# Performance work log

Measured on AMD Instinct MI355X. Metric: run time of the kernel, lower is better.

The kernel has to match this reference:

```python
import jax, jax.numpy as jnp
import numpy as np

B, T, V, E, H, K = 128, 512, 50257, 100, 128, 12
START, STOP = 10, 11


def setup_inputs() -> dict:
    key = jax.random.key(0)
    ks = jax.random.split(key, 11)
    sentences = jax.random.randint(ks[0], (B, T), 0, V)
    h0 = jax.random.normal(ks[1], (B, H), jnp.float32)
    c0 = jax.random.normal(ks[2], (B, H), jnp.float32)
    embed = jax.random.normal(ks[3], (V, E), jnp.float32) * 0.1
    Wih = jax.random.normal(ks[4], (4 * H, E), jnp.float32) * 0.1   # torch gate order i,f,g,o
    Whh = jax.random.normal(ks[5], (4 * H, H), jnp.float32) * 0.1
    bih = jax.random.normal(ks[6], (4 * H,), jnp.float32) * 0.1
    bhh = jax.random.normal(ks[7], (4 * H,), jnp.float32) * 0.1
    Wtag = jax.random.normal(ks[8], (K, H), jnp.float32) * 0.1
    btag = jax.random.normal(ks[9], (K,), jnp.float32) * 0.1
    transitions = jax.random.normal(ks[10], (K, K), jnp.float32)
    transitions = transitions.at[START, :].set(-10000.0).at[:, STOP].set(-10000.0)
    return dict(sentences=sentences, h0=h0, c0=c0, embed=embed,
                Wih=Wih, Whh=Whh, bih=bih, bhh=bhh,
                Wtag=Wtag, btag=btag, transitions=transitions)


def reference(sentences, h0, c0, embed, Wih, Whh, bih, bhh, Wtag, btag, transitions):
    # --- embedding + single-layer LSTM (batch_first); dropout is identity at eval ---
    x = embed[sentences]                       # [B, T, E]
    x_t = jnp.swapaxes(x, 0, 1)                # [T, B, E]

    def lstm_step(carry, xt):
        h, c = carry
        gates = xt @ Wih.T + h @ Whh.T + bih + bhh      # [B, 4H]
        i, f, g, o = jnp.split(gates, 4, axis=-1)
        c = jax.nn.sigmoid(f) * c + jax.nn.sigmoid(i) * jnp.tanh(g)
        h = jax.nn.sigmoid(o) * jnp.tanh(c)
        return (h, c), h

    _, hs = jax.lax.scan(lstm_step, (h0, c0), x_t)      # hs: [T, B, H]
    emissions = hs @ Wtag.T + btag                      # [T, B, K]

    # --- batched Viterbi DP over time ---
    def vit_step(prev, emit):
        # prev: [B, K] trellis at t-1; transitions[i, j] = score(i -> j)
        v = prev[:, :, None] + transitions[None]        # [B, K, K]
        best = jnp.max(v, axis=1)                       # [B, K]
        bp = jnp.argmax(v, axis=1).astype(jnp.int32)    # [B, K]
        return emit + best, bp

    last, bps = jax.lax.scan(vit_step, emissions[0], emissions[1:])  # bps: [T-1, B, K]
    scores = jnp.max(last, axis=-1)                     # [B]
    last_tag = jnp.argmax(last, axis=-1).astype(jnp.int32)  # [B]

    # --- backtrace (reverse scan) ---
    def back_step(tag, bp):
        prev = jnp.take_along_axis(bp, tag[:, None], axis=1)[:, 0]
        return prev, prev

    _, early_tags = jax.lax.scan(back_step, last_tag, bps, reverse=True)  # [T-1, B]
    paths = jnp.concatenate([early_tags, last_tag[None]], axis=0)         # [T, B]
    paths = jnp.swapaxes(paths, 0, 1)                                     # [B, T]
    return scores, paths
```

## Files before the change

### kernel.cpp

```cpp
#include <hip/hip_runtime.h>
#include <hip/hip_bf16.h>

#define BB 128
#define TT 512
#define EE 100
#define HH 128
#define KK 12
#define VV 50257
#define NB 8
#define NBLK 16

typedef short bf16x8 __attribute__((ext_vector_type(8)));
typedef float f32x4  __attribute__((ext_vector_type(4)));

__device__ __forceinline__ unsigned short f2bf(float x) {
  __hip_bfloat16 h = __float2bfloat16(x);
  return *reinterpret_cast<unsigned short*>(&h);
}

__device__ __forceinline__ bf16x8 load8_bf(const float* p) {
  float4 a = *reinterpret_cast<const float4*>(p);
  float4 b = *reinterpret_cast<const float4*>(p + 4);
  bf16x8 r;
  r[0] = (short)f2bf(a.x); r[1] = (short)f2bf(a.y);
  r[2] = (short)f2bf(a.z); r[3] = (short)f2bf(a.w);
  r[4] = (short)f2bf(b.x); r[5] = (short)f2bf(b.y);
  r[6] = (short)f2bf(b.z); r[7] = (short)f2bf(b.w);
  return r;
}

__device__ __forceinline__ bf16x8 load8_bf_pad(const float* row, int k0, int n) {
  bf16x8 r;
  #pragma unroll
  for (int i = 0; i < 8; ++i) {
    unsigned short v = 0;
    if (k0 + i < n) v = f2bf(row[k0 + i]);
    r[i] = (short)v;
  }
  return r;
}

__device__ __forceinline__ float sigr(float x) {
  float e = __builtin_amdgcn_exp2f(x * -1.44269504f);
  return __builtin_amdgcn_rcpf(1.0f + e);
}
__device__ __forceinline__ float tanhr(float x) {
  float e = __builtin_amdgcn_exp2f(x * -2.88539008f);
  return __fmaf_rn(2.0f, __builtin_amdgcn_rcpf(1.0f + e), -1.0f);
}

__device__ __forceinline__ int frag_idx(int b, int k) {
  return ((k >> 5) << 9) + ((b + (((k >> 3) & 3) << 4)) << 3) + (k & 7);
}

__global__ __launch_bounds__(256) void precast_kernel(
    const float* __restrict__ embed, unsigned short* __restrict__ ebf)
{
  int id = blockIdx.x * 256 + threadIdx.x;
  if (id >= VV * 16) return;
  int v = id >> 4, g = id & 15;
  const float* row = embed + (size_t)v * EE;
  bf16x8 o;
  #pragma unroll
  for (int i = 0; i < 8; ++i) {
    int k = g * 8 + i;
    o[i] = (short)((k < EE) ? f2bf(row[k]) : (unsigned short)0);
  }
  *reinterpret_cast<bf16x8*>(ebf + (size_t)id * 8) = o;
}

__global__ __launch_bounds__(512, 2) void lstm_crf_fused(
    const int* __restrict__ sent, const unsigned short* __restrict__ ebf,
    const float* __restrict__ Wih, const float* __restrict__ Whh,
    const float* __restrict__ bih, const float* __restrict__ bhh,
    const float* __restrict__ h0, const float* __restrict__ c0,
    const float* __restrict__ Wtag, const float* __restrict__ btag,
    const float* __restrict__ trans, float* __restrict__ out)
{
  __shared__ unsigned char bp[256 * 96];
  __shared__ int sentl[NB * TT];
  __shared__ __align__(16) unsigned short hfrag[2][2048];
  __shared__ __align__(16) float vit[NB * 16];
  __shared__ __align__(16) float trl[KK * 16];
  __shared__ __align__(16) float ering[2][NB * 16];

  const int bg  = blockIdx.x;
  const int tid = threadIdx.x;
  const int w   = tid >> 6;
  const int l   = tid & 63;
  const int c   = l & 15;
  const int q   = l >> 4;
  const int ew  = 16 * w + c;

  bf16x8 wh[4][4], wx[4][4];
  float biasv[4];
  #pragma unroll
  for (int tt = 0; tt < 4; ++tt) {
    const int gcol = tt * HH + ew;
    biasv[tt] = bih[gcol] + bhh[gcol];
    #pragma unroll
    for (int kt = 0; kt < 4; ++kt) {
      const int k0 = kt * 32 + q * 8;
      wh[tt][kt] = load8_bf(Whh + (size_t)gcol * HH + k0);
      wx[tt][kt] = load8_bf_pad(Wih + (size_t)gcol * EE, k0, EE);
    }
  }

  float cst[2];
  #pragma unroll
  for (int r = 0; r < 2; ++r)
    cst[r] = c0[(size_t)(bg * NB + q * 2 + r) * HH + ew];

  bf16x8 we[4];
  #pragma unroll
  for (int kt = 0; kt < 4; ++kt) {
    #pragma unroll
    for (int i = 0; i < 8; ++i) we[kt][i] = 0;
  }
  float bt = 0.f;
  if (w == 0 && c < KK) {
    #pragma unroll
    for (int kt = 0; kt < 4; ++kt)
      we[kt] = load8_bf(Wtag + (size_t)c * HH + kt * 32 + q * 8);
    bt = btag[c];
  }

  if (tid < 512) {
    int4 z = {0, 0, 0, 0};
    reinterpret_cast<int4*>(hfrag)[tid] = z;
  }
  #pragma unroll
  for (int i = 0; i < NB; ++i) {
    int idx = tid + i * 512;
    sentl[idx] = sent[(size_t)(bg * NB + (idx >> 9)) * TT + (idx & 511)];
  }
  if (tid < KK * KK) {
    int i = tid / KK, jj = tid - i * KK;
    trl[jj * 16 + i] = trans[tid];
  }
  __syncthreads();

  for (int idx = tid; idx < NB * HH; idx += 512) {
    int lb = idx >> 7, k = idx & 127;
    int row = ((lb >> 1) << 2) + (lb & 1);
    hfrag[0][frag_idx(row, k)] = f2bf(h0[(size_t)(bg * NB + lb) * HH + k]);
  }

  const int row  = l & 15;
  const int lbr  = ((row >> 2) << 1) + (row & 1);
  const int koff = (l >> 4) * 8;
  const int* sentr = sent + (size_t)(bg * NB + lbr) * TT;
  bf16x8 xaA[4], xaB[4];
  {
    const bf16x8* s0 = reinterpret_cast<const bf16x8*>(
        ebf + (size_t)sentr[0] * 128 + koff);
    const bf16x8* s1 = reinterpret_cast<const bf16x8*>(
        ebf + (size_t)sentr[1] * 128 + koff);
    #pragma unroll
    for (int kt = 0; kt < 4; ++kt) { xaA[kt] = s0[kt * 4]; xaB[kt] = s1[kt * 4]; }
  }

  const int hw_off = frag_idx(q * 4, ew);
  int nib = 0;
  __syncthreads();

  auto step = [&](int s, bf16x8 (&xcur)[4], bf16x8 (&xnxt)[4]) {
    const int rb = s & 1;
    (void)xnxt;

    bf16x8 ha[4];
    if (s <= TT) {
      const bf16x8* hr = reinterpret_cast<const bf16x8*>(&hfrag[rb][0]) + l;
      #pragma unroll
      for (int kt = 0; kt < 4; ++kt) ha[kt] = hr[kt * 64];
    }

    if (w == 0 && s >= 1 && s <= TT) {
      f32x4 accE = {0.f, 0.f, 0.f, 0.f};
      #pragma unroll
      for (int kt = 0; kt < 4; ++kt)
        accE = __builtin_amdgcn_mfma_f32_16x16x32_bf16(ha[kt], we[kt], accE, 0, 0, 0);
      float* er = &ering[(s - 1) & 1][0];
      #pragma unroll
      for (int r = 0; r < 2; ++r)
        er[(q * 2 + r) * 16 + c] = accE[r] + bt;
    }

    if (s < TT) {
      f32x4 acc[4];
      #pragma unroll
      for (int tt = 0; tt < 4; ++tt) {
        acc[tt][0] = biasv[tt]; acc[tt][1] = biasv[tt];
        acc[tt][2] = biasv[tt]; acc[tt][3] = biasv[tt];
      }
      #pragma unroll
      for (int kt = 0; kt < 4; ++kt) {
        #pragma unroll
        for (int tt = 0; tt < 4; ++tt)
          acc[tt] = __builtin_amdgcn_mfma_f32_16x16x32_bf16(xcur[kt], wx[tt][kt], acc[tt], 0, 0, 0);
      }
      #pragma unroll
      for (int kt = 0; kt < 4; ++kt) {
        #pragma unroll
        for (int tt = 0; tt < 4; ++tt)
          acc[tt] = __builtin_amdgcn_mfma_f32_16x16x32_bf16(ha[kt], wh[tt][kt], acc[tt], 0, 0, 0);
      }

      if (s + 2 < TT) {
        int id = sentl[lbr * TT + s + 2];
        const bf16x8* src = reinterpret_cast<const bf16x8*>(
            ebf + (size_t)id * 128 + koff);
        #pragma unroll
        for (int kt = 0; kt < 4; ++kt) xcur[kt] = src[kt * 4];
      }

      unsigned short* hwp = &hfrag[rb ^ 1][hw_off];
      #pragma unroll
      for (int r = 0; r < 2; ++r) {
        float si = sigr(acc[0][r]);
        float sf = sigr(acc[1][r]);
        float tg = tanhr(acc[2][r]);
        float so = sigr(acc[3][r]);
        cst[r] = __fmaf_rn(sf, cst[r], si * tg);
        hwp[r * 8] = f2bf(so * tanhr(cst[r]));
      }
    }

    if (w >= 4 && s >= 2 && q < 2 && c < KK) {
      const int t_ = s - 2;
      const int b = (w - 4) * 2 + q;
      float Ev = ering[t_ & 1][b * 16 + c];
      float nv;
      if (t_ == 0) {
        nv = Ev;
      } else {
        float4 v0 = *reinterpret_cast<const float4*>(&vit[b * 16]);
        float4 v1 = *reinterpret_cast<const float4*>(&vit[b * 16 + 4]);
        float4 v2 = *reinterpret_cast<const float4*>(&vit[b * 16 + 8]);
        float4 t0 = *reinterpret_cast<const float4*>(&trl[c * 16]);
        float4 t1 = *reinterpret_cast<const float4*>(&trl[c * 16 + 4]);
        float4 t2 = *reinterpret_cast<const float4*>(&trl[c * 16 + 8]);
        float cand[KK] = {v0.x + t0.x, v0.y + t0.y, v0.z + t0.z, v0.w + t0.w,
                          v1.x + t1.x, v1.y + t1.y, v1.z + t1.z, v1.w + t1.w,
                          v2.x + t2.x, v2.y + t2.y, v2.z + t2.z, v2.w + t2.w};
        float g0 = fmaxf(fmaxf(cand[0], cand[1]), cand[2]);
        float g1 = fmaxf(fmaxf(cand[3], cand[4]), cand[5]);
        float g2 = fmaxf(fmaxf(cand[6], cand[7]), cand[8]);
        float g3 = fmaxf(fmaxf(cand[9], cand[10]), cand[11]);
        float best = fmaxf(fmaxf(g0, g1), fmaxf(g2, g3));
        int bi = 11;
        #pragma unroll
        for (int i = 10; i >= 0; --i) bi = (cand[i] == best) ? i : bi;
        nv = Ev + best;
        if (t_ & 1) bp[(t_ >> 1) * 96 + b * 12 + c] =
                        (unsigned char)(nib | (bi << 4));
        else        nib = bi;
      }
      vit[b * 16 + c] = nv;
    }

    __syncthreads();
  };

  for (int s = 0; s < TT + 2; s += 2) {
    step(s, xaA, xaB);
    step(s + 1, xaB, xaA);
  }

  unsigned char* pb = reinterpret_cast<unsigned char*>(hfrag);
  if (tid < NB) {
    int b = tid;
    float best = vit[b * 16];
    int tag = 0;
    for (int jj = 1; jj < KK; ++jj) {
      float v = vit[b * 16 + jj];
      if (v > best) { best = v; tag = jj; }
    }
    out[bg * NB + b] = best;
    pb[b * 512 + 511] = (unsigned char)tag;
    for (int t_ = TT - 1; t_ >= 1; --t_) {
      unsigned char byte = bp[(t_ >> 1) * 96 + b * 12 + tag];
      tag = (t_ & 1) ? (byte >> 4) & 15 : (byte & 15);
      pb[b * 512 + t_ - 1] = (unsigned char)tag;
    }
  }
  __syncthreads();

  #pragma unroll
  for (int i = 0; i < NB; ++i) {
    int idx = tid + i * 512;
    out[BB + (size_t)(bg * NB + (idx >> 9)) * TT + (idx & 511)] = (float)pb[idx];
  }
}

extern "C" void kernel_launch(void* const* d_in, const int* in_sizes, int n_in,
                              void* d_out, int out_size, void* d_ws, size_t ws_size,
                              hipStream_t stream) {
  const int*   sent  = (const int*)d_in[0];
  const float* h0    = (const float*)d_in[1];
  const float* c0    = (const float*)d_in[2];
  const float* embed = (const float*)d_in[3];
  const float* Wih   = (const float*)d_in[4];
  const float* Whh   = (const float*)d_in[5];
  const float* bih   = (const float*)d_in[6];
  const float* bhh   = (const float*)d_in[7];
  const float* Wtag  = (const float*)d_in[8];
  const float* btag  = (const float*)d_in[9];
  const float* trans = (const float*)d_in[10];
  float* out = (float*)d_out;
  unsigned short* ebf = (unsigned short*)d_ws;

  precast_kernel<<<(VV * 16 + 255) / 256, 256, 0, stream>>>(embed, ebf);
  lstm_crf_fused<<<NBLK, 512, 0, stream>>>(
      sent, ebf, Wih, Whh, bih, bhh, h0, c0, Wtag, btag, trans, out);
}
```

Baseline: 561.0 us.

## Halve batch rows per block, fold bias into embedding MFMA, lighten step barrier

Each block now handles 4 sequences instead of 8 and the grid doubles to 32 blocks. This spreads the serial LSTM/Viterbi recurrence over more CUs and shortens each thread's per-step gate epilogue to a single row. The LSTM bias is folded into the input MFMA through a constant-1 column at position 100 of the padded bf16 embedding, so the bias-init registers go away. The per-step __syncthreads is replaced by a raw lgkmcnt wait plus s_barrier. The cost is that MFMA tiles are now mostly padding (only 4 of 16 rows used), the bias is rounded to bf16, and the barrier change depends on no global-memory ordering being needed across steps.

```diff
diff --git a/kernel.cpp b/kernel.cpp
--- a/kernel.cpp
+++ b/kernel.cpp
@@ -7,8 +7,8 @@
 #define HH 128
 #define KK 12
 #define VV 50257
-#define NB 8
-#define NBLK 16
+#define NB 4
+#define NBLK 32
 
 typedef short bf16x8 __attribute__((ext_vector_type(8)));
 typedef float f32x4  __attribute__((ext_vector_type(4)));
@@ -29,12 +29,15 @@
   return r;
 }
 
-__device__ __forceinline__ bf16x8 load8_bf_pad(const float* row, int k0, int n) {
+__device__ __forceinline__ bf16x8 load8_bf_pad_bias(const float* row, int k0,
+                                                    float bias) {
   bf16x8 r;
   #pragma unroll
   for (int i = 0; i < 8; ++i) {
+    int k = k0 + i;
     unsigned short v = 0;
-    if (k0 + i < n) v = f2bf(row[k0 + i]);
+    if (k < EE) v = f2bf(row[k]);
+    else if (k == EE) v = f2bf(bias);
     r[i] = (short)v;
   }
   return r;
@@ -51,6 +54,10 @@
 
 __device__ __forceinline__ int frag_idx(int b, int k) {
   return ((k >> 5) << 9) + ((b + (((k >> 3) & 3) << 4)) << 3) + (k & 7);
+}
+
+__device__ __forceinline__ void lds_barrier() {
+  asm volatile("s_waitcnt lgkmcnt(0)\n\ts_barrier" ::: "memory");
 }
 
 __global__ __launch_bounds__(256) void precast_kernel(
@@ -64,7 +71,10 @@
   #pragma unroll
   for (int i = 0; i < 8; ++i) {
     int k = g * 8 + i;
-    o[i] = (short)((k < EE) ? f2bf(row[k]) : (unsigned short)0);
+    unsigned short u = 0;
+    if (k < EE) u = f2bf(row[k]);
+    else if (k == EE) u = 0x3F80;
+    o[i] = (short)u;
   }
   *reinterpret_cast<bf16x8*>(ebf + (size_t)id * 8) = o;
 }
@@ -77,7 +87,7 @@
     const float* __restrict__ Wtag, const float* __restrict__ btag,
     const float* __restrict__ trans, float* __restrict__ out)
 {
-  __shared__ unsigned char bp[256 * 96];
+  __shared__ unsigned char bp[256 * (NB * 12)];
   __shared__ int sentl[NB * TT];
   __shared__ __align__(16) unsigned short hfrag[2][2048];
   __shared__ __align__(16) float vit[NB * 16];
@@ -93,23 +103,19 @@
   const int ew  = 16 * w + c;
 
   bf16x8 wh[4][4], wx[4][4];
-  float biasv[4];
   #pragma unroll
   for (int tt = 0; tt < 4; ++tt) {
     const int gcol = tt * HH + ew;
-    biasv[tt] = bih[gcol] + bhh[gcol];
+    const float bias = bih[gcol] + bhh[gcol];
     #pragma unroll
     for (int kt = 0; kt < 4; ++kt) {
       const int k0 = kt * 32 + q * 8;
       wh[tt][kt] = load8_bf(Whh + (size_t)gcol * HH + k0);
-      wx[tt][kt] = load8_bf_pad(Wih + (size_t)gcol * EE, k0, EE);
-    }
-  }
-
-  float cst[2];
-  #pragma unroll
-  for (int r = 0; r < 2; ++r)
-    cst[r] = c0[(size_t)(bg * NB + q * 2 + r) * HH + ew];
+      wx[tt][kt] = load8_bf_pad_bias(Wih + (size_t)gcol * EE, k0, bias);
+    }
+  }
+
+  float cst = c0[(size_t)(bg * NB + q) * HH + ew];
 
   bf16x8 we[4];
   #pragma unroll
@@ -125,7 +131,7 @@
     bt = btag[c];
   }
 
-  if (tid < 512) {
+  {
     int4 z = {0, 0, 0, 0};
     reinterpret_cast<int4*>(hfrag)[tid] = z;
   }
@@ -140,14 +146,12 @@
   }
   __syncthreads();
 
-  for (int idx = tid; idx < NB * HH; idx += 512) {
-    int lb = idx >> 7, k = idx & 127;
-    int row = ((lb >> 1) << 2) + (lb & 1);
-    hfrag[0][frag_idx(row, k)] = f2bf(h0[(size_t)(bg * NB + lb) * HH + k]);
-  }
-
-  const int row  = l & 15;
-  const int lbr  = ((row >> 2) << 1) + (row & 1);
+  if (tid < NB * HH) {
+    int lb = tid >> 7, k = tid & 127;
+    hfrag[0][frag_idx(lb * 4, k)] = f2bf(h0[(size_t)(bg * NB + lb) * HH + k]);
+  }
+
+  const int lbr  = c >> 2;
   const int koff = (l >> 4) * 8;
   const int* sentr = sent + (size_t)(bg * NB + lbr) * TT;
   bf16x8 xaA[4], xaB[4];
@@ -164,9 +168,8 @@
   int nib = 0;
   __syncthreads();
 
-  auto step = [&](int s, bf16x8 (&xcur)[4], bf16x8 (&xnxt)[4]) {
+  auto step = [&](int s, bf16x8 (&xcur)[4]) {
     const int rb = s & 1;
-    (void)xnxt;
 
     bf16x8 ha[4];
     if (s <= TT) {
@@ -180,18 +183,15 @@
       #pragma unroll
       for (int kt = 0; kt < 4; ++kt)
         accE = __builtin_amdgcn_mfma_f32_16x16x32_bf16(ha[kt], we[kt], accE, 0, 0, 0);
-      float* er = &ering[(s - 1) & 1][0];
-      #pragma unroll
-      for (int r = 0; r < 2; ++r)
-        er[(q * 2 + r) * 16 + c] = accE[r] + bt;
+      ering[(s - 1) & 1][q * 16 + c] = accE[0] + bt;
     }
 
     if (s < TT) {
       f32x4 acc[4];
       #pragma unroll
       for (int tt = 0; tt < 4; ++tt) {
-        acc[tt][0] = biasv[tt]; acc[tt][1] = biasv[tt];
-        acc[tt][2] = biasv[tt]; acc[tt][3] = biasv[tt];
+        f32x4 z = {0.f, 0.f, 0.f, 0.f};
+        acc[tt] = z;
       }
       #pragma unroll
       for (int kt = 0; kt < 4; ++kt) {
@@ -214,21 +214,17 @@
         for (int kt = 0; kt < 4; ++kt) xcur[kt] = src[kt * 4];
       }
 
-      unsigned short* hwp = &hfrag[rb ^ 1][hw_off];
-      #pragma unroll
-      for (int r = 0; r < 2; ++r) {
-        float si = sigr(acc[0][r]);
-        float sf = sigr(acc[1][r]);
-        float tg = tanhr(acc[2][r]);
-        float so = sigr(acc[3][r]);
-        cst[r] = __fmaf_rn(sf, cst[r], si * tg);
-        hwp[r * 8] = f2bf(so * tanhr(cst[r]));
-      }
-    }
-
-    if (w >= 4 && s >= 2 && q < 2 && c < KK) {
+      float si = sigr(acc[0][0]);
+      float sf = sigr(acc[1][0]);
+      float tg = tanhr(acc[2][0]);
+      float so = sigr(acc[3][0]);
+      cst = __fmaf_rn(sf, cst, si * tg);
+      hfrag[rb ^ 1][hw_off] = f2bf(so * tanhr(cst));
+    }
+
+    if (w >= 4 && s >= 2 && q == 0 && c < KK) {
       const int t_ = s - 2;
-      const int b = (w - 4) * 2 + q;
+      const int b = w - 4;
       float Ev = ering[t_ & 1][b * 16 + c];
       float nv;
       if (t_ == 0) {
@@ -252,20 +248,21 @@
         #pragma unroll
         for (int i = 10; i >= 0; --i) bi = (cand[i] == best) ? i : bi;
         nv = Ev + best;
-        if (t_ & 1) bp[(t_ >> 1) * 96 + b * 12 + c] =
+        if (t_ & 1) bp[(t_ >> 1) * (NB * 12) + b * 12 + c] =
                         (unsigned char)(nib | (bi << 4));
         else        nib = bi;
       }
       vit[b * 16 + c] = nv;
     }
 
-    __syncthreads();
+    lds_barrier();
   };
 
   for (int s = 0; s < TT + 2; s += 2) {
-    step(s, xaA, xaB);
-    step(s + 1, xaB, xaA);
-  }
+    step(s, xaA);
+    step(s + 1, xaB);
+  }
+  __syncthreads();
 
   unsigned char* pb = reinterpret_cast<unsigned char*>(hfrag);
   if (tid < NB) {
@@ -279,7 +276,7 @@
     out[bg * NB + b] = best;
     pb[b * 512 + 511] = (unsigned char)tag;
     for (int t_ = TT - 1; t_ >= 1; --t_) {
-      unsigned char byte = bp[(t_ >> 1) * 96 + b * 12 + tag];
+      unsigned char byte = bp[(t_ >> 1) * (NB * 12) + b * 12 + tag];
       tag = (t_ & 1) ? (byte >> 4) & 15 : (byte & 15);
       pb[b * 512 + t_ - 1] = (unsigned char)tag;
     }
```

After: 635.8 us. +13.3%, slower.

## Precompute input-projection gates in a parallel kernel before the recurrent LSTM loop

Applied to the files above, without the earlier changes.

The x·Wih + bias input projection is pulled out of the sequential recurrence into a separate, fully parallel MFMA kernel. It writes bf16 pre-gates for every (batch, time) pair, with the bias folded in through a constant-one embedding column. The recurrent kernel then loads four pre-gate values per step instead of gathering embeddings and running 16 extra MFMAs on the critical path. In exchange it adds two kernel launches, a global round trip for the pre-gates, an extra bf16 rounding of the gate inputs, and 56 KB of dynamic shared-memory padding.

```diff
diff --git a/kernel.cpp b/kernel.cpp
--- a/kernel.cpp
+++ b/kernel.cpp
@@ -16,6 +16,9 @@
 __device__ __forceinline__ unsigned short f2bf(float x) {
   __hip_bfloat16 h = __float2bfloat16(x);
   return *reinterpret_cast<unsigned short*>(&h);
+}
+__device__ __forceinline__ float bf2f(unsigned short u) {
+  return __uint_as_float(((unsigned)u) << 16);
 }
 
 __device__ __forceinline__ bf16x8 load8_bf(const float* p) {
@@ -29,12 +32,15 @@
   return r;
 }
 
-__device__ __forceinline__ bf16x8 load8_bf_pad(const float* row, int k0, int n) {
+__device__ __forceinline__ bf16x8 load8_bf_pad_bias(const float* row, int k0,
+                                                    float bias) {
   bf16x8 r;
   #pragma unroll
   for (int i = 0; i < 8; ++i) {
+    int k = k0 + i;
     unsigned short v = 0;
-    if (k0 + i < n) v = f2bf(row[k0 + i]);
+    if (k < EE) v = f2bf(row[k]);
+    else if (k == EE) v = f2bf(bias);
     r[i] = (short)v;
   }
   return r;
@@ -64,25 +70,85 @@
   #pragma unroll
   for (int i = 0; i < 8; ++i) {
     int k = g * 8 + i;
-    o[i] = (short)((k < EE) ? f2bf(row[k]) : (unsigned short)0);
+    unsigned short u = 0;
+    if (k < EE) u = f2bf(row[k]);
+    else if (k == EE) u = 0x3F80;
+    o[i] = (short)u;
   }
   *reinterpret_cast<bf16x8*>(ebf + (size_t)id * 8) = o;
 }
 
+__global__ __launch_bounds__(256) void wprep_kernel(
+    const float* __restrict__ Wih, const float* __restrict__ bih,
+    const float* __restrict__ bhh, unsigned short* __restrict__ wbf)
+{
+  int id = blockIdx.x * 256 + threadIdx.x;
+  if (id >= 8 * 4 * 4 * 64) return;
+  int l = id & 63, kt = (id >> 6) & 3, tt = (id >> 8) & 3, s8 = id >> 10;
+  int gcol = tt * HH + 16 * s8 + (l & 15);
+  int k0 = kt * 32 + (l >> 4) * 8;
+  float bias = bih[gcol] + bhh[gcol];
+  bf16x8 r = load8_bf_pad_bias(Wih + (size_t)gcol * EE, k0, bias);
+  *reinterpret_cast<bf16x8*>(wbf + (size_t)id * 8) = r;
+}
+
+__global__ __launch_bounds__(256, 2) void pregates_kernel(
+    const int* __restrict__ sent, const unsigned short* __restrict__ ebf,
+    const unsigned short* __restrict__ wbf, unsigned short* __restrict__ P16)
+{
+  const int w = threadIdx.x >> 6, l = threadIdx.x & 63;
+  const int c = l & 15, q = l >> 4;
+  const int rt = blockIdx.x * 4 + w;
+  const int flat = rt * 16 + c;
+  const int b = flat >> 9, t = flat & 511;
+  const int id = sent[b * TT + t];
+
+  bf16x8 xa[4];
+  #pragma unroll
+  for (int kt = 0; kt < 4; ++kt)
+    xa[kt] = *reinterpret_cast<const bf16x8*>(
+        ebf + (size_t)id * 128 + kt * 32 + q * 8);
+
+  const bf16x8* wb = reinterpret_cast<const bf16x8*>(wbf);
+  #pragma unroll
+  for (int s8 = 0; s8 < 8; ++s8) {
+    f32x4 acc[4];
+    #pragma unroll
+    for (int tt = 0; tt < 4; ++tt) {
+      f32x4 z = {0.f, 0.f, 0.f, 0.f};
+      acc[tt] = z;
+    }
+    #pragma unroll
+    for (int kt = 0; kt < 4; ++kt) {
+      #pragma unroll
+      for (int tt = 0; tt < 4; ++tt)
+        acc[tt] = __builtin_amdgcn_mfma_f32_16x16x32_bf16(
+            xa[kt], wb[((s8 * 4 + tt) * 4 + kt) * 64 + l], acc[tt], 0, 0, 0);
+    }
+    const int e = s8 * 16 + c;
+    #pragma unroll
+    for (int r4 = 0; r4 < 4; ++r4) {
+      int fr = rt * 16 + q * 4 + r4;
+      ushort4 o = make_ushort4(f2bf(acc[0][r4]), f2bf(acc[1][r4]),
+                               f2bf(acc[2][r4]), f2bf(acc[3][r4]));
+      *reinterpret_cast<ushort4*>(P16 + ((size_t)fr * 128 + e) * 4) = o;
+    }
+  }
+}
+
 __global__ __launch_bounds__(512, 2) void lstm_crf_fused(
-    const int* __restrict__ sent, const unsigned short* __restrict__ ebf,
-    const float* __restrict__ Wih, const float* __restrict__ Whh,
-    const float* __restrict__ bih, const float* __restrict__ bhh,
+    const unsigned short* __restrict__ P16, const float* __restrict__ Whh,
     const float* __restrict__ h0, const float* __restrict__ c0,
     const float* __restrict__ Wtag, const float* __restrict__ btag,
     const float* __restrict__ trans, float* __restrict__ out)
 {
-  __shared__ unsigned char bp[256 * 96];
-  __shared__ int sentl[NB * TT];
+  __shared__ unsigned char bp[256 * (NB * 12)];
   __shared__ __align__(16) unsigned short hfrag[2][2048];
   __shared__ __align__(16) float vit[NB * 16];
   __shared__ __align__(16) float trl[KK * 16];
   __shared__ __align__(16) float ering[2][NB * 16];
+  extern __shared__ char dynpad[];
+  (void)dynpad;
 
   const int bg  = blockIdx.x;
   const int tid = threadIdx.x;
@@ -92,18 +158,13 @@
   const int q   = l >> 4;
   const int ew  = 16 * w + c;
 
-  bf16x8 wh[4][4], wx[4][4];
-  float biasv[4];
+  bf16x8 wh[4][4];
   #pragma unroll
   for (int tt = 0; tt < 4; ++tt) {
     const int gcol = tt * HH + ew;
-    biasv[tt] = bih[gcol] + bhh[gcol];
-    #pragma unroll
-    for (int kt = 0; kt < 4; ++kt) {
-      const int k0 = kt * 32 + q * 8;
-      wh[tt][kt] = load8_bf(Whh + (size_t)gcol * HH + k0);
-      wx[tt][kt] = load8_bf_pad(Wih + (size_t)gcol * EE, k0, EE);
-    }
+    #pragma unroll
+    for (int kt = 0; kt < 4; ++kt)
+      wh[tt][kt] = load8_bf(Whh + (size_t)gcol * HH + kt * 32 + q * 8);
   }
 
   float cst[2];
@@ -125,14 +186,9 @@
     bt = btag[c];
   }
 
-  if (tid < 512) {
+  {
     int4 z = {0, 0, 0, 0};
     reinterpret_cast<int4*>(hfrag)[tid] = z;
-  }
-  #pragma unroll
-  for (int i = 0; i < NB; ++i) {
-    int idx = tid + i * 512;
-    sentl[idx] = sent[(size_t)(bg * NB + (idx >> 9)) * TT + (idx & 511)];
   }
   if (tid < KK * KK) {
     int i = tid / KK, jj = tid - i * KK;
@@ -146,27 +202,22 @@
     hfrag[0][frag_idx(row, k)] = f2bf(h0[(size_t)(bg * NB + lb) * HH + k]);
   }
 
-  const int row  = l & 15;
-  const int lbr  = ((row >> 2) << 1) + (row & 1);
-  const int koff = (l >> 4) * 8;
-  const int* sentr = sent + (size_t)(bg * NB + lbr) * TT;
-  bf16x8 xaA[4], xaB[4];
-  {
-    const bf16x8* s0 = reinterpret_cast<const bf16x8*>(
-        ebf + (size_t)sentr[0] * 128 + koff);
-    const bf16x8* s1 = reinterpret_cast<const bf16x8*>(
-        ebf + (size_t)sentr[1] * 128 + koff);
-    #pragma unroll
-    for (int kt = 0; kt < 4; ++kt) { xaA[kt] = s0[kt * 4]; xaB[kt] = s1[kt * 4]; }
-  }
+  const unsigned short* pb0 =
+      P16 + (size_t)(bg * NB + q * 2 + 0) * (TT * 512) + ew * 4;
+  const unsigned short* pb1 =
+      P16 + (size_t)(bg * NB + q * 2 + 1) * (TT * 512) + ew * 4;
+  ushort4 pA[2], pB[2];
+  pA[0] = *reinterpret_cast<const ushort4*>(pb0);
+  pA[1] = *reinterpret_cast<const ushort4*>(pb1);
+  pB[0] = *reinterpret_cast<const ushort4*>(pb0 + 512);
+  pB[1] = *reinterpret_cast<const ushort4*>(pb1 + 512);
 
   const int hw_off = frag_idx(q * 4, ew);
   int nib = 0;
   __syncthreads();
 
-  auto step = [&](int s, bf16x8 (&xcur)[4], bf16x8 (&xnxt)[4]) {
+  auto step = [&](int s, ushort4 (&pcur)[2]) {
     const int rb = s & 1;
-    (void)xnxt;
 
     bf16x8 ha[4];
     if (s <= TT) {
@@ -175,43 +226,28 @@
       for (int kt = 0; kt < 4; ++kt) ha[kt] = hr[kt * 64];
     }
 
-    if (w == 0 && s >= 1 && s <= TT) {
-      f32x4 accE = {0.f, 0.f, 0.f, 0.f};
-      #pragma unroll
-      for (int kt = 0; kt < 4; ++kt)
-        accE = __builtin_amdgcn_mfma_f32_16x16x32_bf16(ha[kt], we[kt], accE, 0, 0, 0);
-      float* er = &ering[(s - 1) & 1][0];
-      #pragma unroll
-      for (int r = 0; r < 2; ++r)
-        er[(q * 2 + r) * 16 + c] = accE[r] + bt;
-    }
-
     if (s < TT) {
       f32x4 acc[4];
       #pragma unroll
       for (int tt = 0; tt < 4; ++tt) {
-        acc[tt][0] = biasv[tt]; acc[tt][1] = biasv[tt];
-        acc[tt][2] = biasv[tt]; acc[tt][3] = biasv[tt];
-      }
-      #pragma unroll
-      for (int kt = 0; kt < 4; ++kt) {
-        #pragma unroll
-        for (int tt = 0; tt < 4; ++tt)
-          acc[tt] = __builtin_amdgcn_mfma_f32_16x16x32_bf16(xcur[kt], wx[tt][kt], acc[tt], 0, 0, 0);
-      }
+        f32x4 z = {0.f, 0.f, 0.f, 0.f};
+        acc[tt] = z;
+      }
+      acc[0][0] = bf2f(pcur[0].x); acc[1][0] = bf2f(pcur[0].y);
+      acc[2][0] = bf2f(pcur[0].z); acc[3][0] = bf2f(pcur[0].w);
+      acc[0][1] = bf2f(pcur[1].x); acc[1][1] = bf2f(pcur[1].y);
+      acc[2][1] = bf2f(pcur[1].z); acc[3][1] = bf2f(pcur[1].w);
+
+      if (s + 2 < TT) {
+        pcur[0] = *reinterpret_cast<const ushort4*>(pb0 + (size_t)(s + 2) * 512);
+        pcur[1] = *reinterpret_cast<const ushort4*>(pb1 + (size_t)(s + 2) * 512);
+      }
+
       #pragma unroll
       for (int kt = 0; kt < 4; ++kt) {
         #pragma unroll
         for (int tt = 0; tt < 4; ++tt)
           acc[tt] = __builtin_amdgcn_mfma_f32_16x16x32_bf16(ha[kt], wh[tt][kt], acc[tt], 0, 0, 0);
-      }
-
-      if (s + 2 < TT) {
-        int id = sentl[lbr * TT + s + 2];
-        const bf16x8* src = reinterpret_cast<const bf16x8*>(
-            ebf + (size_t)id * 128 + koff);
-        #pragma unroll
-        for (int kt = 0; kt < 4; ++kt) xcur[kt] = src[kt * 4];
       }
 
       unsigned short* hwp = &hfrag[rb ^ 1][hw_off];
@@ -224,6 +260,18 @@
         cst[r] = __fmaf_rn(sf, cst[r], si * tg);
         hwp[r * 8] = f2bf(so * tanhr(cst[r]));
       }
+    } else if (s + 2 < TT) {
+    }
+
+    if (w == 0 && s >= 1 && s <= TT) {
+      f32x4 accE = {0.f, 0.f, 0.f, 0.f};
+      #pragma unroll
+      for (int kt = 0; kt < 4; ++kt)
+        accE = __builtin_amdgcn_mfma_f32_16x16x32_bf16(ha[kt], we[kt], accE, 0, 0, 0);
+      float* er = &ering[(s - 1) & 1][0];
+      #pragma unroll
+      for (int r = 0; r < 2; ++r)
+        er[(q * 2 + r) * 16 + c] = accE[r] + bt;
     }
 
     if (w >= 4 && s >= 2 && q < 2 && c < KK) {
@@ -252,7 +300,7 @@
         #pragma unroll
         for (int i = 10; i >= 0; --i) bi = (cand[i] == best) ? i : bi;
         nv = Ev + best;
-        if (t_ & 1) bp[(t_ >> 1) * 96 + b * 12 + c] =
+        if (t_ & 1) bp[(t_ >> 1) * (NB * 12) + b * 12 + c] =
                         (unsigned char)(nib | (bi << 4));
         else        nib = bi;
       }
@@ -263,8 +311,8 @@
   };
 
   for (int s = 0; s < TT + 2; s += 2) {
-    step(s, xaA, xaB);
-    step(s + 1, xaB, xaA);
+    step(s, pA);
+    step(s + 1, pB);
   }
 
   unsigned char* pb = reinterpret_cast<unsigned char*>(hfrag);
@@ -279,7 +327,7 @@
     out[bg * NB + b] = best;
     pb[b * 512 + 511] = (unsigned char)tag;
     for (int t_ = TT - 1; t_ >= 1; --t_) {
-      unsigned char byte = bp[(t_ >> 1) * 96 + b * 12 + tag];
+      unsigned char byte = bp[(t_ >> 1) * (NB * 12) + b * 12 + tag];
       tag = (t_ & 1) ? (byte >> 4) & 15 : (byte & 15);
       pb[b * 512 + t_ - 1] = (unsigned char)tag;
     }
@@ -308,9 +356,14 @@
   const float* btag  = (const float*)d_in[9];
   const float* trans = (const float*)d_in[10];
   float* out = (float*)d_out;
+
   unsigned short* ebf = (unsigned short*)d_ws;
+  unsigned short* wbf = ebf + (size_t)VV * 128;
+  unsigned short* P16 = wbf + 8192 * 8;
 
   precast_kernel<<<(VV * 16 + 255) / 256, 256, 0, stream>>>(embed, ebf);
-  lstm_crf_fused<<<NBLK, 512, 0, stream>>>(
-      sent, ebf, Wih, Whh, bih, bhh, h0, c0, Wtag, btag, trans, out);
-}
+  wprep_kernel<<<32, 256, 0, stream>>>(Wih, bih, bhh, wbf);
+  pregates_kernel<<<(BB * TT / 16) / 4, 256, 0, stream>>>(sent, ebf, wbf, P16);
+  lstm_crf_fused<<<NBLK, 512, 56 * 1024, stream>>>(
+      P16, Whh, h0, c0, Wtag, btag, trans, out);
+}
```

Result: faster. 536.1 us (-4.4%).
